# Optimization experiments

Measured on AMD Instinct MI355X. Metric: run time of the kernel, lower is better.

Reference implementation:

```python
import jax, jax.numpy as jnp
import numpy as np

B, N, D, H = 4, 2048, 256, 8
d = D // H          # 32 per-head dim
EPS = 1e-5
SCALE = 1.0 / float(np.sqrt(d))


def setup_inputs() -> dict:
    key = jax.random.key(0)
    ks = jax.random.split(key, 6)
    s = 0.02
    x = jax.random.normal(ks[0], (B, N, D), jnp.float32)
    # RoPE frequencies: theta_j = 10000^(-2j/d), angle = pos * theta
    inv_freq = 1.0 / (10000.0 ** (jnp.arange(0, d, 2, dtype=jnp.float32) / d))  # (d/2,)
    ang = jnp.arange(N, dtype=jnp.float32)[:, None] * inv_freq[None, :]          # (N, d/2)
    return {
        "x": x,
        "freqs_cos": jnp.cos(ang),
        "freqs_sin": jnp.sin(ang),
        "w_qkv": jax.random.normal(ks[1], (D, 3 * D), jnp.float32) * s,
        "b_qkv": jnp.zeros((3 * D,), jnp.float32),
        "w_proj": jax.random.normal(ks[2], (D, D), jnp.float32) * s,
        "b_proj": jnp.zeros((D,), jnp.float32),
        "ln1_g": jnp.ones((D,), jnp.float32),
        "ln1_b": jnp.zeros((D,), jnp.float32),
        "ln2_g": jnp.ones((D,), jnp.float32),
        "ln2_b": jnp.zeros((D,), jnp.float32),
        "w1": jax.random.normal(ks[3], (D, 2 * D), jnp.float32) * s,
        "b1": jnp.zeros((2 * D,), jnp.float32),
        "w2": jax.random.normal(ks[4], (2 * D, D), jnp.float32) * s,
        "b2": jnp.zeros((D,), jnp.float32),
    }


def _layer_norm(x, g, b):
    mu = jnp.mean(x, axis=-1, keepdims=True)
    var = jnp.mean(jnp.square(x - mu), axis=-1, keepdims=True)
    return (x - mu) * jax.lax.rsqrt(var + EPS) * g + b


def _rope(t, cos, sin):
    # t: (B,H,N,d); interleaved (even,odd) pairs viewed as complex, multiplied by e^{i*ang}
    tr = t.reshape(B, H, N, d // 2, 2)
    te, to = tr[..., 0], tr[..., 1]
    c = cos[None, None, :, :]
    s = sin[None, None, :, :]
    oe = te * c - to * s
    oo = te * s + to * c
    return jnp.stack([oe, oo], axis=-1).reshape(B, H, N, d)


def reference(x, freqs_cos, freqs_sin, w_qkv, b_qkv, w_proj, b_proj,
              ln1_g, ln1_b, ln2_g, ln2_b, w1, b1, w2, b2):
    # Pre-LN MHSA with RoPE (dropout = identity at eval)
    h = _layer_norm(x, ln1_g, ln1_b)
    qkv = (h @ w_qkv + b_qkv).reshape(B, N, 3, H, d).transpose(0, 2, 3, 1, 4)  # (B,3,H,N,d)
    q, k, v = qkv[:, 0], qkv[:, 1], qkv[:, 2]
    q = _rope(q, freqs_cos, freqs_sin)
    k = _rope(k, freqs_cos, freqs_sin)
    attn = jax.nn.softmax(jnp.einsum('bhnd,bhmd->bhnm', q, k) * SCALE, axis=-1)
    out = jnp.einsum('bhnm,bhmd->bhnd', attn, v).transpose(0, 2, 1, 3).reshape(B, N, D)
    x = x + (out @ w_proj + b_proj)
    h = _layer_norm(x, ln2_g, ln2_b)
    ffn = jax.nn.relu(h @ w1 + b1) @ w2 + b2
    return x + ffn
```

## Files before the change

kernel.cpp:

```cpp
#include <hip/hip_runtime.h>
#include <hip/hip_bf16.h>
#include <math.h>

#define Bsz 4
#define Nseq 2048
#define Dm 256
#define Hh 8
#define Hd 32
#define EPS_ 1e-5f
#define SCALE_ 0.17677669529663687f
#define QSC_ (0.17677669529663687f * 1.4426950408889634f)

typedef __attribute__((ext_vector_type(8))) short short8;
typedef __attribute__((ext_vector_type(4))) short short4v;
typedef __attribute__((ext_vector_type(4))) float f32x4;
typedef __attribute__((ext_vector_type(16))) float f32x16;

__device__ __forceinline__ void gload16(const void* g, void* l) {
    __builtin_amdgcn_global_load_lds(
        (const __attribute__((address_space(1))) void*)g,
        (__attribute__((address_space(3))) void*)l, 16, 0, 0);
}

__device__ __forceinline__ short bf16s(float f) {
    __hip_bfloat16 h = __float2bfloat16(f);
    return *(short*)&h;
}

union FU { float f; unsigned u; };

__device__ __forceinline__ int pk2bf(float a, float b) {
    FU ua, ub; ua.f = a; ub.f = b;
    return (int)__builtin_amdgcn_perm(ub.u, ua.u, 0x07060302u);
}

union I4S8 { int i[4]; short8 s; };

__global__ __launch_bounds__(256) void ln_kernel(const float* __restrict__ x,
                                                 const float* __restrict__ g,
                                                 const float* __restrict__ b,
                                                 __hip_bfloat16* __restrict__ out) {
    int row  = blockIdx.x * 4 + (threadIdx.x >> 6);
    int lane = threadIdx.x & 63;
    const float* xr = x + (size_t)row * Dm;
    float4 v = *(const float4*)(xr + lane * 4);
    float s  = v.x + v.y + v.z + v.w;
    float ss = v.x * v.x + v.y * v.y + v.z * v.z + v.w * v.w;
    #pragma unroll
    for (int off = 32; off; off >>= 1) {
        s  += __shfl_xor(s, off);
        ss += __shfl_xor(ss, off);
    }
    float mu  = s * (1.0f / Dm);
    float var = ss * (1.0f / Dm) - mu * mu;
    float rs  = rsqrtf(var + EPS_);
    float4 gv = *(const float4*)(g + lane * 4);
    float4 bv = *(const float4*)(b + lane * 4);
    short4v o4 = { bf16s((v.x - mu) * rs * gv.x + bv.x),
                   bf16s((v.y - mu) * rs * gv.y + bv.y),
                   bf16s((v.z - mu) * rs * gv.z + bv.z),
                   bf16s((v.w - mu) * rs * gv.w + bv.w) };
    *(short4v*)(out + (size_t)row * Dm + lane * 4) = o4;
}

__global__ __launch_bounds__(256) void wconv_kernel(
    const float* __restrict__ s0, const float* __restrict__ s1,
    const float* __restrict__ s2, const float* __restrict__ s3,
    __hip_bfloat16* __restrict__ d0, __hip_bfloat16* __restrict__ d1,
    __hip_bfloat16* __restrict__ d2, __hip_bfloat16* __restrict__ d3) {
    __shared__ float t[32][33];
    int bid = blockIdx.x;
    const float* src; __hip_bfloat16* dst; int K, N, tb;
    if (bid < 192)      { src = s0; dst = d0; K = 256; N = 768; tb = bid; }
    else if (bid < 256) { src = s1; dst = d1; K = 256; N = 256; tb = bid - 192; }
    else if (bid < 384) { src = s2; dst = d2; K = 256; N = 512; tb = bid - 256; }
    else                { src = s3; dst = d3; K = 512; N = 256; tb = bid - 384; }
    int tn = N >> 5;
    int k0 = (tb / tn) * 32, n0 = (tb % tn) * 32;
    int c = threadIdx.x & 31, r0 = threadIdx.x >> 5;
    #pragma unroll
    for (int i = 0; i < 4; i++) {
        int r = r0 + i * 8;
        t[r][c] = src[(size_t)(k0 + r) * N + n0 + c];
    }
    __syncthreads();
    #pragma unroll
    for (int i = 0; i < 4; i++) {
        int n = r0 + i * 8;
        dst[(size_t)(n0 + n) * K + k0 + c] = __float2bfloat16(t[c][n]);
    }
}

template <int TM, int EPI>
__global__ __launch_bounds__(256) void mfma_gemm(const __hip_bfloat16* __restrict__ A,
                                                 const __hip_bfloat16* __restrict__ Wt,
                                                 const float* __restrict__ bias,
                                                 const float* __restrict__ res,
                                                 float* __restrict__ Cf,
                                                 __hip_bfloat16* __restrict__ Cb,
                                                 int M, int Nn, int K) {
    constexpr int MF = TM / 64;
    __shared__ __align__(16) __hip_bfloat16 As[TM * 32];
    __shared__ __align__(16) __hip_bfloat16 Bs[64 * 32];
    const int tid = threadIdx.x, w = tid >> 6, lane = tid & 63;
    const int lm = lane & 15, lq = lane >> 4;
    const int bm = blockIdx.y * TM, bn = blockIdx.x * 64;
    f32x4 acc[MF][4];
    #pragma unroll
    for (int i = 0; i < MF; i++)
        #pragma unroll
        for (int j = 0; j < 4; j++) acc[i][j] = (f32x4){0.f, 0.f, 0.f, 0.f};

    const int sw = (lq ^ (lm & 3)) * 8;
    for (int k0 = 0; k0 < K; k0 += 32) {
        #pragma unroll
        for (int p = 0; p < MF; p++) {
            int c = p * 256 + tid;
            int r = c >> 2, gk = ((c & 3) ^ (r & 3)) * 8;
            gload16(A + (size_t)(bm + r) * K + k0 + gk, As + (p * 256 + w * 64) * 8);
        }
        {
            int r = tid >> 2, gk = ((tid & 3) ^ (r & 3)) * 8;
            gload16(Wt + (size_t)(bn + r) * K + k0 + gk, Bs + w * 512);
        }
        __syncthreads();
        short8 a[MF];
        #pragma unroll
        for (int mf = 0; mf < MF; mf++)
            a[mf] = *(const short8*)&As[(w * (TM / 4) + mf * 16 + lm) * 32 + sw];
        #pragma unroll
        for (int nf = 0; nf < 4; nf++) {
            short8 bfr = *(const short8*)&Bs[(nf * 16 + lm) * 32 + sw];
            #pragma unroll
            for (int mf = 0; mf < MF; mf++)
                acc[mf][nf] = __builtin_amdgcn_mfma_f32_16x16x32_bf16(a[mf], bfr, acc[mf][nf], 0, 0, 0);
        }
        __syncthreads();
    }
    #pragma unroll
    for (int nf = 0; nf < 4; nf++) {
        int cg = bn + nf * 16 + lm;
        float bi = bias[cg];
        #pragma unroll
        for (int mf = 0; mf < MF; mf++) {
            #pragma unroll
            for (int r = 0; r < 4; r++) {
                int rg = bm + w * (TM / 4) + mf * 16 + lq * 4 + r;
                float v = acc[mf][nf][r] + bi;
                if (EPI == 1) {
                    v = fmaxf(v, 0.f);
                    Cb[(size_t)rg * Nn + cg] = __float2bfloat16(v);
                } else {
                    v += res[(size_t)rg * Nn + cg];
                    Cf[(size_t)rg * Nn + cg] = v;
                }
            }
        }
    }
}

__global__ __launch_bounds__(256) void qkv_mfma(const __hip_bfloat16* __restrict__ A,
                                                const __hip_bfloat16* __restrict__ Wt,
                                                const float* __restrict__ bias,
                                                const float* __restrict__ fcos,
                                                const float* __restrict__ fsin,
                                                __hip_bfloat16* __restrict__ qout,
                                                __hip_bfloat16* __restrict__ kout,
                                                __hip_bfloat16* __restrict__ vt) {
    const int K = 256, Nn = 768;
    __shared__ __align__(16) __hip_bfloat16 As[128 * 32];
    __shared__ __align__(16) __hip_bfloat16 Bs[64 * 32];
    const int tid = threadIdx.x, w = tid >> 6, lane = tid & 63;
    const int lm = lane & 15, lq = lane >> 4;
    const int bm = blockIdx.y * 128, bn = blockIdx.x * 64;
    f32x4 acc[2][4];
    #pragma unroll
    for (int i = 0; i < 2; i++)
        #pragma unroll
        for (int j = 0; j < 4; j++) acc[i][j] = (f32x4){0.f, 0.f, 0.f, 0.f};

    const int sw = (lq ^ (lm & 3)) * 8;
    for (int k0 = 0; k0 < K; k0 += 32) {
        #pragma unroll
        for (int p = 0; p < 2; p++) {
            int c = p * 256 + tid;
            int r = c >> 2, gk = ((c & 3) ^ (r & 3)) * 8;
            gload16(A + (size_t)(bm + r) * K + k0 + gk, As + (p * 256 + w * 64) * 8);
        }
        {
            int r = tid >> 2, gk = ((tid & 3) ^ (r & 3)) * 8;
            gload16(Wt + (size_t)(bn + r) * K + k0 + gk, Bs + w * 512);
        }
        __syncthreads();
        short8 a0 = *(const short8*)&As[(w * 32 + lm) * 32 + sw];
        short8 a1 = *(const short8*)&As[(w * 32 + 16 + lm) * 32 + sw];
        #pragma unroll
        for (int nf = 0; nf < 4; nf++) {
            short8 bfr = *(const short8*)&Bs[(nf * 16 + lm) * 32 + sw];
            acc[0][nf] = __builtin_amdgcn_mfma_f32_16x16x32_bf16(a0, bfr, acc[0][nf], 0, 0, 0);
            acc[1][nf] = __builtin_amdgcn_mfma_f32_16x16x32_bf16(a1, bfr, acc[1][nf], 0, 0, 0);
        }
        __syncthreads();
    }
    const int seg = bn >> 8;
    #pragma unroll
    for (int nf = 0; nf < 4; nf++) {
        int cg = bn + nf * 16 + lm;
        int hh = (cg & 255) >> 5;
        int dd = (nf & 1) * 16 + lm;
        int i0 = dd >> 1;
        float bi = bias[cg];
        #pragma unroll
        for (int mf = 0; mf < 2; mf++) {
            #pragma unroll
            for (int r = 0; r < 4; r++) {
                int rg = bm + w * 32 + mf * 16 + lq * 4 + r;
                int bb = rg >> 11, n = rg & (Nseq - 1);
                float v = acc[mf][nf][r] + bi;
                if (seg == 2) {
                    vt[(((size_t)(bb * Hh + hh)) * Hd + dd) * Nseq + n] = __float2bfloat16(v);
                } else {
                    float vp = __shfl_xor(v, 1);
                    float cs = fcos[n * 16 + i0], sn = fsin[n * 16 + i0];
                    float outv = (dd & 1) ? (vp * sn + v * cs) : (v * cs - vp * sn);
                    if (seg == 0) outv *= QSC_;
                    __hip_bfloat16* dst = (seg == 0) ? qout : kout;
                    dst[(((size_t)(bb * Hh + hh)) * Nseq + n) * Hd + dd] = __float2bfloat16(outv);
                }
            }
        }
    }
}

__global__ __launch_bounds__(256) void attn_mfma(const __hip_bfloat16* __restrict__ q,
                                                 const __hip_bfloat16* __restrict__ k,
                                                 const __hip_bfloat16* __restrict__ vt,
                                                 __hip_bfloat16* __restrict__ att) {
    __shared__ __align__(16) char smem[4096 + 16384 + 16384 + 512];
    __hip_bfloat16* Qs  = (__hip_bfloat16*)smem;
    __hip_bfloat16* KsB = (__hip_bfloat16*)(smem + 4096);
    __hip_bfloat16* VsB = (__hip_bfloat16*)(smem + 20480);
    float* RedO = (float*)(smem + 4096);
    float* RedS = (float*)(smem + 4096 + 8192);
    float* smS  = (float*)(smem + 4096 + 8192 + 256);

    const int tid = threadIdx.x, w = tid >> 6, lane = tid & 63;
    const int l31 = lane & 31, hi = lane >> 5;
    const int wq = w >> 1, wk = w & 1;
    const int bh = blockIdx.y, qbase = blockIdx.x * 64;
    const __hip_bfloat16* qp = q + ((size_t)bh * Nseq + qbase) * Hd;
    const __hip_bfloat16* kp = k + (size_t)bh * Nseq * Hd;
    const __hip_bfloat16* vp = vt + (size_t)bh * Hd * Nseq;
    const int r8 = tid >> 3, s8 = tid & 7;

    {
        int r = tid >> 2, sl = tid & 3;
        gload16(qp + r * 32 + ((sl ^ (r & 3)) * 8), Qs + w * 512);
    }
    #pragma unroll
    for (int par = 0; par < 2; par++) {
        gload16(kp + (par * 64 + 2 * r8 + (s8 >> 2)) * 32 + (((s8 & 3) ^ (r8 & 3)) * 8),
                KsB + par * 2048 + w * 512);
        gload16(vp + (size_t)r8 * Nseq + par * 64 + ((s8 ^ (r8 & 7)) * 8),
                VsB + par * 2048 + w * 512);
    }
    __syncthreads();

    const int qrow = wq * 32 + l31;
    short8 qf0 = *(const short8*)&Qs[qrow * 32 + ((hi ^ (l31 & 3)) * 8)];
    short8 qf1 = *(const short8*)&Qs[qrow * 32 + (((2 + hi) ^ (l31 & 3)) * 8)];

    f32x16 O;
    #pragma unroll
    for (int i = 0; i < 16; i++) O[i] = 0.f;
    float sm = 0.f;

    for (int t = 0; t < 16; t++) {
        const int buf = t & 1;
        if (t + 1 < 16) {
            const int kb2 = (t + 1) * 128;
            #pragma unroll
            for (int par = 0; par < 2; par++) {
                gload16(kp + (kb2 + par * 64 + 2 * r8 + (s8 >> 2)) * 32 + (((s8 & 3) ^ (r8 & 3)) * 8),
                        KsB + ((buf ^ 1) * 2 + par) * 2048 + w * 512);
                gload16(vp + (size_t)r8 * Nseq + kb2 + par * 64 + ((s8 ^ (r8 & 7)) * 8),
                        VsB + ((buf ^ 1) * 2 + par) * 2048 + w * 512);
            }
        }
        const __hip_bfloat16* Kc = KsB + (buf * 2 + wk) * 2048;
        const __hip_bfloat16* Vc = VsB + (buf * 2 + wk) * 2048;
        f32x16 St0, St1;
        #pragma unroll
        for (int i = 0; i < 16; i++) { St0[i] = 0.f; St1[i] = 0.f; }
        {
            int pr = l31 >> 1, elb = pr * 64 + (l31 & 1) * 32;
            short8 kf0 = *(const short8*)&Kc[elb + ((hi ^ (pr & 3)) * 8)];
            short8 kf1 = *(const short8*)&Kc[elb + (((2 + hi) ^ (pr & 3)) * 8)];
            St0 = __builtin_amdgcn_mfma_f32_32x32x16_bf16(kf0, qf0, St0, 0, 0, 0);
            St0 = __builtin_amdgcn_mfma_f32_32x32x16_bf16(kf1, qf1, St0, 0, 0, 0);
        }
        {
            int pr = 16 + (l31 >> 1), elb = pr * 64 + (l31 & 1) * 32;
            short8 kf0 = *(const short8*)&Kc[elb + ((hi ^ (pr & 3)) * 8)];
            short8 kf1 = *(const short8*)&Kc[elb + (((2 + hi) ^ (pr & 3)) * 8)];
            St1 = __builtin_amdgcn_mfma_f32_32x32x16_bf16(kf0, qf0, St1, 0, 0, 0);
            St1 = __builtin_amdgcn_mfma_f32_32x32x16_bf16(kf1, qf1, St1, 0, 0, 0);
        }
        int pk0[8], pk1[8];
        #pragma unroll
        for (int p = 0; p < 8; p++) {
            float a = __builtin_amdgcn_exp2f(St0[2 * p]);
            float b = __builtin_amdgcn_exp2f(St0[2 * p + 1]);
            sm += a + b;
            pk0[p] = pk2bf(a, b);
        }
        #pragma unroll
        for (int p = 0; p < 8; p++) {
            float a = __builtin_amdgcn_exp2f(St1[2 * p]);
            float b = __builtin_amdgcn_exp2f(St1[2 * p + 1]);
            sm += a + b;
            pk1[p] = pk2bf(a, b);
        }
        #pragma unroll
        for (int tt = 0; tt < 4; tt++) {
            const int* PK = (tt >> 1) ? pk1 : pk0;
            const int base = 4 * (tt & 1);
            int keep0 = hi ? PK[base + 2] : PK[base + 0];
            int keep1 = hi ? PK[base + 3] : PK[base + 1];
            int send0 = hi ? PK[base + 0] : PK[base + 2];
            int send1 = hi ? PK[base + 1] : PK[base + 3];
            int x0 = __shfl_xor(send0, 32);
            int x1 = __shfl_xor(send1, 32);
            I4S8 u;
            u.i[0] = hi ? x0 : keep0;
            u.i[1] = hi ? x1 : keep1;
            u.i[2] = hi ? keep0 : x0;
            u.i[3] = hi ? keep1 : x1;
            short8 vf = *(const short8*)&Vc[l31 * 64 + (((2 * tt + hi) ^ (l31 & 7)) * 8)];
            O = __builtin_amdgcn_mfma_f32_32x32x16_bf16(u.s, vf, O, 0, 0, 0);
        }
        __syncthreads();
    }
    sm += __shfl_xor(sm, 32);
    if (wk == 1) {
        #pragma unroll
        for (int j = 0; j < 16; j++) RedO[(wq * 16 + j) * 64 + lane] = O[j];
        if (hi == 0) RedS[wq * 32 + l31] = sm;
    }
    __syncthreads();
    if (wk == 0) {
        #pragma unroll
        for (int j = 0; j < 16; j++) O[j] += RedO[(wq * 16 + j) * 64 + lane];
        sm += RedS[wq * 32 + l31];
        if (hi == 0) smS[wq * 32 + l31] = sm;
    }
    __syncthreads();
    if (wk == 0) {
        const int bb = bh >> 3, hh = bh & 7;
        #pragma unroll
        for (int m = 0; m < 4; m++) {
            float4 sv = *(const float4*)&smS[wq * 32 + 8 * m + 4 * hi];
            #pragma unroll
            for (int i = 0; i < 4; i++) {
                int n = qbase + wq * 32 + 8 * m + 4 * hi + i;
                att[((size_t)(bb * Nseq + n)) * Dm + hh * Hd + l31] =
                    __float2bfloat16(O[4 * m + i] * (1.0f / sv[i]));
            }
        }
    }
}

extern "C" void kernel_launch(void* const* d_in, const int* in_sizes, int n_in,
                              void* d_out, int out_size, void* d_ws, size_t ws_size,
                              hipStream_t stream) {
    const float* x      = (const float*)d_in[0];
    const float* fcos   = (const float*)d_in[1];
    const float* fsin   = (const float*)d_in[2];
    const float* w_qkv  = (const float*)d_in[3];
    const float* b_qkv  = (const float*)d_in[4];
    const float* w_proj = (const float*)d_in[5];
    const float* b_proj = (const float*)d_in[6];
    const float* ln1_g  = (const float*)d_in[7];
    const float* ln1_b  = (const float*)d_in[8];
    const float* ln2_g  = (const float*)d_in[9];
    const float* ln2_b  = (const float*)d_in[10];
    const float* w1     = (const float*)d_in[11];
    const float* b1     = (const float*)d_in[12];
    const float* w2     = (const float*)d_in[13];
    const float* b2     = (const float*)d_in[14];
    float* out = (float*)d_out;
    char* base = (char*)d_ws;
    const size_t MB = (size_t)1 << 20;

    __hip_bfloat16* h   = (__hip_bfloat16*)(base);
    __hip_bfloat16* qb  = (__hip_bfloat16*)(base + 4 * MB);
    __hip_bfloat16* kbf = (__hip_bfloat16*)(base + 8 * MB);
    __hip_bfloat16* vtb = (__hip_bfloat16*)(base + 12 * MB);
    __hip_bfloat16* att = (__hip_bfloat16*)(base + 16 * MB);
    float*          x2f = (float*)(base + 20 * MB);
    __hip_bfloat16* h2  = (__hip_bfloat16*)(base);
    __hip_bfloat16* ffn = (__hip_bfloat16*)(base + 28 * MB);
    __hip_bfloat16* wqT = (__hip_bfloat16*)(base + 40 * MB);
    __hip_bfloat16* wpT = (__hip_bfloat16*)(base + 40 * MB + 393216);
    __hip_bfloat16* w1T = (__hip_bfloat16*)(base + 40 * MB + 524288);
    __hip_bfloat16* w2T = (__hip_bfloat16*)(base + 40 * MB + 786432);

    const int rows = Bsz * Nseq;

    wconv_kernel<<<512, 256, 0, stream>>>(w_qkv, w_proj, w1, w2, wqT, wpT, w1T, w2T);
    ln_kernel<<<rows / 4, 256, 0, stream>>>(x, ln1_g, ln1_b, h);
    qkv_mfma<<<dim3(12, 64), 256, 0, stream>>>(h, wqT, b_qkv, fcos, fsin, qb, kbf, vtb);
    attn_mfma<<<dim3(Nseq / 64, Bsz * Hh), 256, 0, stream>>>(qb, kbf, vtb, att);
    mfma_gemm<64, 2><<<dim3(4, 128), 256, 0, stream>>>(att, wpT, b_proj, x, x2f, nullptr,
                                                       rows, 256, 256);
    ln_kernel<<<rows / 4, 256, 0, stream>>>(x2f, ln2_g, ln2_b, h2);
    mfma_gemm<128, 1><<<dim3(8, 64), 256, 0, stream>>>(h2, w1T, b1, nullptr, nullptr, ffn,
                                                       rows, 512, 256);
    mfma_gemm<64, 2><<<dim3(4, 128), 256, 0, stream>>>(ffn, w2T, b2, x2f, out, nullptr,
                                                       rows, 256, 512);
}
```

Baseline: 184.5 us.

## Double-buffer GEMM LDS tiles with K=64 steps and fuse LN1 with weight conversion

Both GEMM kernels now take K-steps of 64 with double-buffered LDS tiles, an 8-way XOR swizzle and a single barrier per iteration. The next tile's loads are issued before the current tile's MFMAs, so global load latency can be hidden. The M tile is fixed at 64, which doubles the grid for the QKV and FFN1 GEMMs. The first LayerNorm and the weight transpose/convert kernel are merged into one launch to cut launch overhead. The trade-off is more LDS per block and less reuse of each weight tile across rows.

```diff
diff --git a/kernel.cpp b/kernel.cpp
--- a/kernel.cpp
+++ b/kernel.cpp
@@ -35,6 +35,60 @@
 }
 
 union I4S8 { int i[4]; short8 s; };
+
+__global__ __launch_bounds__(256) void prep_kernel(
+    const float* __restrict__ x, const float* __restrict__ g1,
+    const float* __restrict__ b1v, __hip_bfloat16* __restrict__ hout,
+    const float* __restrict__ s0, const float* __restrict__ s1,
+    const float* __restrict__ s2, const float* __restrict__ s3,
+    __hip_bfloat16* __restrict__ d0, __hip_bfloat16* __restrict__ d1,
+    __hip_bfloat16* __restrict__ d2, __hip_bfloat16* __restrict__ d3) {
+    __shared__ float t[32][33];
+    if (blockIdx.x < 2048) {
+        int row  = blockIdx.x * 4 + (threadIdx.x >> 6);
+        int lane = threadIdx.x & 63;
+        const float* xr = x + (size_t)row * Dm;
+        float4 v = *(const float4*)(xr + lane * 4);
+        float s  = v.x + v.y + v.z + v.w;
+        float ss = v.x * v.x + v.y * v.y + v.z * v.z + v.w * v.w;
+        #pragma unroll
+        for (int off = 32; off; off >>= 1) {
+            s  += __shfl_xor(s, off);
+            ss += __shfl_xor(ss, off);
+        }
+        float mu  = s * (1.0f / Dm);
+        float var = ss * (1.0f / Dm) - mu * mu;
+        float rs  = rsqrtf(var + EPS_);
+        float4 gv = *(const float4*)(g1 + lane * 4);
+        float4 bv = *(const float4*)(b1v + lane * 4);
+        short4v o4 = { bf16s((v.x - mu) * rs * gv.x + bv.x),
+                       bf16s((v.y - mu) * rs * gv.y + bv.y),
+                       bf16s((v.z - mu) * rs * gv.z + bv.z),
+                       bf16s((v.w - mu) * rs * gv.w + bv.w) };
+        *(short4v*)(hout + (size_t)row * Dm + lane * 4) = o4;
+        return;
+    }
+    int bid = blockIdx.x - 2048;
+    const float* src; __hip_bfloat16* dst; int K, N, tb;
+    if (bid < 192)      { src = s0; dst = d0; K = 256; N = 768; tb = bid; }
+    else if (bid < 256) { src = s1; dst = d1; K = 256; N = 256; tb = bid - 192; }
+    else if (bid < 384) { src = s2; dst = d2; K = 256; N = 512; tb = bid - 256; }
+    else                { src = s3; dst = d3; K = 512; N = 256; tb = bid - 384; }
+    int tn = N >> 5;
+    int k0 = (tb / tn) * 32, n0 = (tb % tn) * 32;
+    int c = threadIdx.x & 31, r0 = threadIdx.x >> 5;
+    #pragma unroll
+    for (int i = 0; i < 4; i++) {
+        int r = r0 + i * 8;
+        t[r][c] = src[(size_t)(k0 + r) * N + n0 + c];
+    }
+    __syncthreads();
+    #pragma unroll
+    for (int i = 0; i < 4; i++) {
+        int n = r0 + i * 8;
+        dst[(size_t)(n0 + n) * K + k0 + c] = __float2bfloat16(t[c][n]);
+    }
+}
 
 __global__ __launch_bounds__(256) void ln_kernel(const float* __restrict__ x,
                                                  const float* __restrict__ g,
@@ -63,35 +117,7 @@
     *(short4v*)(out + (size_t)row * Dm + lane * 4) = o4;
 }
 
-__global__ __launch_bounds__(256) void wconv_kernel(
-    const float* __restrict__ s0, const float* __restrict__ s1,
-    const float* __restrict__ s2, const float* __restrict__ s3,
-    __hip_bfloat16* __restrict__ d0, __hip_bfloat16* __restrict__ d1,
-    __hip_bfloat16* __restrict__ d2, __hip_bfloat16* __restrict__ d3) {
-    __shared__ float t[32][33];
-    int bid = blockIdx.x;
-    const float* src; __hip_bfloat16* dst; int K, N, tb;
-    if (bid < 192)      { src = s0; dst = d0; K = 256; N = 768; tb = bid; }
-    else if (bid < 256) { src = s1; dst = d1; K = 256; N = 256; tb = bid - 192; }
-    else if (bid < 384) { src = s2; dst = d2; K = 256; N = 512; tb = bid - 256; }
-    else                { src = s3; dst = d3; K = 512; N = 256; tb = bid - 384; }
-    int tn = N >> 5;
-    int k0 = (tb / tn) * 32, n0 = (tb % tn) * 32;
-    int c = threadIdx.x & 31, r0 = threadIdx.x >> 5;
-    #pragma unroll
-    for (int i = 0; i < 4; i++) {
-        int r = r0 + i * 8;
-        t[r][c] = src[(size_t)(k0 + r) * N + n0 + c];
-    }
-    __syncthreads();
-    #pragma unroll
-    for (int i = 0; i < 4; i++) {
-        int n = r0 + i * 8;
-        dst[(size_t)(n0 + n) * K + k0 + c] = __float2bfloat16(t[c][n]);
-    }
-}
-
-template <int TM, int EPI>
+template <int EPI>
 __global__ __launch_bounds__(256) void mfma_gemm(const __hip_bfloat16* __restrict__ A,
                                                  const __hip_bfloat16* __restrict__ Wt,
                                                  const float* __restrict__ bias,
@@ -99,61 +125,62 @@
                                                  float* __restrict__ Cf,
                                                  __hip_bfloat16* __restrict__ Cb,
                                                  int M, int Nn, int K) {
-    constexpr int MF = TM / 64;
-    __shared__ __align__(16) __hip_bfloat16 As[TM * 32];
-    __shared__ __align__(16) __hip_bfloat16 Bs[64 * 32];
+    __shared__ __align__(16) __hip_bfloat16 As[2][64 * 64];
+    __shared__ __align__(16) __hip_bfloat16 Bs[2][64 * 64];
     const int tid = threadIdx.x, w = tid >> 6, lane = tid & 63;
     const int lm = lane & 15, lq = lane >> 4;
-    const int bm = blockIdx.y * TM, bn = blockIdx.x * 64;
-    f32x4 acc[MF][4];
-    #pragma unroll
-    for (int i = 0; i < MF; i++)
-        #pragma unroll
-        for (int j = 0; j < 4; j++) acc[i][j] = (f32x4){0.f, 0.f, 0.f, 0.f};
-
-    const int sw = (lq ^ (lm & 3)) * 8;
-    for (int k0 = 0; k0 < K; k0 += 32) {
-        #pragma unroll
-        for (int p = 0; p < MF; p++) {
-            int c = p * 256 + tid;
-            int r = c >> 2, gk = ((c & 3) ^ (r & 3)) * 8;
-            gload16(A + (size_t)(bm + r) * K + k0 + gk, As + (p * 256 + w * 64) * 8);
-        }
-        {
-            int r = tid >> 2, gk = ((tid & 3) ^ (r & 3)) * 8;
-            gload16(Wt + (size_t)(bn + r) * K + k0 + gk, Bs + w * 512);
-        }
+    const int bm = blockIdx.y * 64, bn = blockIdx.x * 64;
+    f32x4 acc[4];
+    #pragma unroll
+    for (int j = 0; j < 4; j++) acc[j] = (f32x4){0.f, 0.f, 0.f, 0.f};
+
+    const int sr = tid >> 3, ssl = tid & 7;
+    const int sgk = (ssl ^ (sr & 7)) * 8;
+    const int sr2 = 32 + sr;
+    const int sgk2 = (ssl ^ (sr2 & 7)) * 8;
+
+    gload16(A + (size_t)(bm + sr) * K + sgk, &As[0][w * 512]);
+    gload16(A + (size_t)(bm + sr2) * K + sgk2, &As[0][2048 + w * 512]);
+    gload16(Wt + (size_t)(bn + sr) * K + sgk, &Bs[0][w * 512]);
+    gload16(Wt + (size_t)(bn + sr2) * K + sgk2, &Bs[0][2048 + w * 512]);
+
+    const int arow = w * 16 + lm;
+    const int ar7 = arow & 7, cr7base = lm & 7;
+    for (int t = 0; t < K / 64; t++) {
+        const int buf = t & 1;
         __syncthreads();
-        short8 a[MF];
-        #pragma unroll
-        for (int mf = 0; mf < MF; mf++)
-            a[mf] = *(const short8*)&As[(w * (TM / 4) + mf * 16 + lm) * 32 + sw];
-        #pragma unroll
-        for (int nf = 0; nf < 4; nf++) {
-            short8 bfr = *(const short8*)&Bs[(nf * 16 + lm) * 32 + sw];
+        if (t + 1 < K / 64) {
+            int k0 = (t + 1) * 64;
+            gload16(A + (size_t)(bm + sr) * K + k0 + sgk, &As[buf ^ 1][w * 512]);
+            gload16(A + (size_t)(bm + sr2) * K + k0 + sgk2, &As[buf ^ 1][2048 + w * 512]);
+            gload16(Wt + (size_t)(bn + sr) * K + k0 + sgk, &Bs[buf ^ 1][w * 512]);
+            gload16(Wt + (size_t)(bn + sr2) * K + k0 + sgk2, &Bs[buf ^ 1][2048 + w * 512]);
+        }
+        #pragma unroll
+        for (int ks = 0; ks < 2; ks++) {
+            short8 a = *(const short8*)&As[buf][arow * 64 + (((ks * 4 + lq) ^ ar7) * 8)];
             #pragma unroll
-            for (int mf = 0; mf < MF; mf++)
-                acc[mf][nf] = __builtin_amdgcn_mfma_f32_16x16x32_bf16(a[mf], bfr, acc[mf][nf], 0, 0, 0);
-        }
-        __syncthreads();
+            for (int nf = 0; nf < 4; nf++) {
+                int cc = nf * 16 + lm;
+                short8 bfr = *(const short8*)&Bs[buf][cc * 64 + (((ks * 4 + lq) ^ (cc & 7)) * 8)];
+                acc[nf] = __builtin_amdgcn_mfma_f32_16x16x32_bf16(a, bfr, acc[nf], 0, 0, 0);
+            }
+        }
     }
     #pragma unroll
     for (int nf = 0; nf < 4; nf++) {
         int cg = bn + nf * 16 + lm;
         float bi = bias[cg];
         #pragma unroll
-        for (int mf = 0; mf < MF; mf++) {
-            #pragma unroll
-            for (int r = 0; r < 4; r++) {
-                int rg = bm + w * (TM / 4) + mf * 16 + lq * 4 + r;
-                float v = acc[mf][nf][r] + bi;
-                if (EPI == 1) {
-                    v = fmaxf(v, 0.f);
-                    Cb[(size_t)rg * Nn + cg] = __float2bfloat16(v);
-                } else {
-                    v += res[(size_t)rg * Nn + cg];
-                    Cf[(size_t)rg * Nn + cg] = v;
-                }
+        for (int r = 0; r < 4; r++) {
+            int rg = bm + w * 16 + lq * 4 + r;
+            float v = acc[nf][r] + bi;
+            if (EPI == 1) {
+                v = fmaxf(v, 0.f);
+                Cb[(size_t)rg * Nn + cg] = __float2bfloat16(v);
+            } else {
+                v += res[(size_t)rg * Nn + cg];
+                Cf[(size_t)rg * Nn + cg] = v;
             }
         }
     }
@@ -167,40 +194,48 @@
                                                 __hip_bfloat16* __restrict__ qout,
                                                 __hip_bfloat16* __restrict__ kout,
                                                 __hip_bfloat16* __restrict__ vt) {
-    const int K = 256, Nn = 768;
-    __shared__ __align__(16) __hip_bfloat16 As[128 * 32];
-    __shared__ __align__(16) __hip_bfloat16 Bs[64 * 32];
+    const int K = 256;
+    __shared__ __align__(16) __hip_bfloat16 As[2][64 * 64];
+    __shared__ __align__(16) __hip_bfloat16 Bs[2][64 * 64];
     const int tid = threadIdx.x, w = tid >> 6, lane = tid & 63;
     const int lm = lane & 15, lq = lane >> 4;
-    const int bm = blockIdx.y * 128, bn = blockIdx.x * 64;
-    f32x4 acc[2][4];
-    #pragma unroll
-    for (int i = 0; i < 2; i++)
-        #pragma unroll
-        for (int j = 0; j < 4; j++) acc[i][j] = (f32x4){0.f, 0.f, 0.f, 0.f};
-
-    const int sw = (lq ^ (lm & 3)) * 8;
-    for (int k0 = 0; k0 < K; k0 += 32) {
-        #pragma unroll
-        for (int p = 0; p < 2; p++) {
-            int c = p * 256 + tid;
-            int r = c >> 2, gk = ((c & 3) ^ (r & 3)) * 8;
-            gload16(A + (size_t)(bm + r) * K + k0 + gk, As + (p * 256 + w * 64) * 8);
-        }
-        {
-            int r = tid >> 2, gk = ((tid & 3) ^ (r & 3)) * 8;
-            gload16(Wt + (size_t)(bn + r) * K + k0 + gk, Bs + w * 512);
-        }
+    const int bm = blockIdx.y * 64, bn = blockIdx.x * 64;
+    f32x4 acc[4];
+    #pragma unroll
+    for (int j = 0; j < 4; j++) acc[j] = (f32x4){0.f, 0.f, 0.f, 0.f};
+
+    const int sr = tid >> 3, ssl = tid & 7;
+    const int sgk = (ssl ^ (sr & 7)) * 8;
+    const int sr2 = 32 + sr;
+    const int sgk2 = (ssl ^ (sr2 & 7)) * 8;
+
+    gload16(A + (size_t)(bm + sr) * K + sgk, &As[0][w * 512]);
+    gload16(A + (size_t)(bm + sr2) * K + sgk2, &As[0][2048 + w * 512]);
+    gload16(Wt + (size_t)(bn + sr) * K + sgk, &Bs[0][w * 512]);
+    gload16(Wt + (size_t)(bn + sr2) * K + sgk2, &Bs[0][2048 + w * 512]);
+
+    const int arow = w * 16 + lm;
+    const int ar7 = arow & 7;
+    for (int t = 0; t < K / 64; t++) {
+        const int buf = t & 1;
         __syncthreads();
-        short8 a0 = *(const short8*)&As[(w * 32 + lm) * 32 + sw];
-        short8 a1 = *(const short8*)&As[(w * 32 + 16 + lm) * 32 + sw];
-        #pragma unroll
-        for (int nf = 0; nf < 4; nf++) {
-            short8 bfr = *(const short8*)&Bs[(nf * 16 + lm) * 32 + sw];
-            acc[0][nf] = __builtin_amdgcn_mfma_f32_16x16x32_bf16(a0, bfr, acc[0][nf], 0, 0, 0);
-            acc[1][nf] = __builtin_amdgcn_mfma_f32_16x16x32_bf16(a1, bfr, acc[1][nf], 0, 0, 0);
-        }
-        __syncthreads();
+        if (t + 1 < K / 64) {
+            int k0 = (t + 1) * 64;
+            gload16(A + (size_t)(bm + sr) * K + k0 + sgk, &As[buf ^ 1][w * 512]);
+            gload16(A + (size_t)(bm + sr2) * K + k0 + sgk2, &As[buf ^ 1][2048 + w * 512]);
+            gload16(Wt + (size_t)(bn + sr) * K + k0 + sgk, &Bs[buf ^ 1][w * 512]);
+            gload16(Wt + (size_t)(bn + sr2) * K + k0 + sgk2, &Bs[buf ^ 1][2048 + w * 512]);
+        }
+        #pragma unroll
+        for (int ks = 0; ks < 2; ks++) {
+            short8 a = *(const short8*)&As[buf][arow * 64 + (((ks * 4 + lq) ^ ar7) * 8)];
+            #pragma unroll
+            for (int nf = 0; nf < 4; nf++) {
+                int cc = nf * 16 + lm;
+                short8 bfr = *(const short8*)&Bs[buf][cc * 64 + (((ks * 4 + lq) ^ (cc & 7)) * 8)];
+                acc[nf] = __builtin_amdgcn_mfma_f32_16x16x32_bf16(a, bfr, acc[nf], 0, 0, 0);
+            }
+        }
     }
     const int seg = bn >> 8;
     #pragma unroll
@@ -211,22 +246,19 @@
         int i0 = dd >> 1;
         float bi = bias[cg];
         #pragma unroll
-        for (int mf = 0; mf < 2; mf++) {
-            #pragma unroll
-            for (int r = 0; r < 4; r++) {
-                int rg = bm + w * 32 + mf * 16 + lq * 4 + r;
-                int bb = rg >> 11, n = rg & (Nseq - 1);
-                float v = acc[mf][nf][r] + bi;
-                if (seg == 2) {
-                    vt[(((size_t)(bb * Hh + hh)) * Hd + dd) * Nseq + n] = __float2bfloat16(v);
-                } else {
-                    float vp = __shfl_xor(v, 1);
-                    float cs = fcos[n * 16 + i0], sn = fsin[n * 16 + i0];
-                    float outv = (dd & 1) ? (vp * sn + v * cs) : (v * cs - vp * sn);
-                    if (seg == 0) outv *= QSC_;
-                    __hip_bfloat16* dst = (seg == 0) ? qout : kout;
-                    dst[(((size_t)(bb * Hh + hh)) * Nseq + n) * Hd + dd] = __float2bfloat16(outv);
-                }
+        for (int r = 0; r < 4; r++) {
+            int rg = bm + w * 16 + lq * 4 + r;
+            int bb = rg >> 11, n = rg & (Nseq - 1);
+            float v = acc[nf][r] + bi;
+            if (seg == 2) {
+                vt[(((size_t)(bb * Hh + hh)) * Hd + dd) * Nseq + n] = __float2bfloat16(v);
+            } else {
+                float vp = __shfl_xor(v, 1);
+                float cs = fcos[n * 16 + i0], sn = fsin[n * 16 + i0];
+                float outv = (dd & 1) ? (vp * sn + v * cs) : (v * cs - vp * sn);
+                if (seg == 0) outv *= QSC_;
+                __hip_bfloat16* dst = (seg == 0) ? qout : kout;
+                dst[(((size_t)(bb * Hh + hh)) * Nseq + n) * Hd + dd] = __float2bfloat16(outv);
             }
         }
     }
@@ -407,15 +439,15 @@
 
     const int rows = Bsz * Nseq;
 
-    wconv_kernel<<<512, 256, 0, stream>>>(w_qkv, w_proj, w1, w2, wqT, wpT, w1T, w2T);
-    ln_kernel<<<rows / 4, 256, 0, stream>>>(x, ln1_g, ln1_b, h);
-    qkv_mfma<<<dim3(12, 64), 256, 0, stream>>>(h, wqT, b_qkv, fcos, fsin, qb, kbf, vtb);
+    prep_kernel<<<2560, 256, 0, stream>>>(x, ln1_g, ln1_b, h,
+                                          w_qkv, w_proj, w1, w2, wqT, wpT, w1T, w2T);
+    qkv_mfma<<<dim3(12, 128), 256, 0, stream>>>(h, wqT, b_qkv, fcos, fsin, qb, kbf, vtb);
     attn_mfma<<<dim3(Nseq / 64, Bsz * Hh), 256, 0, stream>>>(qb, kbf, vtb, att);
-    mfma_gemm<64, 2><<<dim3(4, 128), 256, 0, stream>>>(att, wpT, b_proj, x, x2f, nullptr,
-                                                       rows, 256, 256);
+    mfma_gemm<2><<<dim3(4, 128), 256, 0, stream>>>(att, wpT, b_proj, x, x2f, nullptr,
+                                                   rows, 256, 256);
     ln_kernel<<<rows / 4, 256, 0, stream>>>(x2f, ln2_g, ln2_b, h2);
-    mfma_gemm<128, 1><<<dim3(8, 64), 256, 0, stream>>>(h2, w1T, b1, nullptr, nullptr, ffn,
-                                                       rows, 512, 256);
-    mfma_gemm<64, 2><<<dim3(4, 128), 256, 0, stream>>>(ffn, w2T, b2, x2f, out, nullptr,
-                                                       rows, 256, 512);
-}
+    mfma_gemm<1><<<dim3(8, 128), 256, 0, stream>>>(h2, w1T, b1, nullptr, nullptr, ffn,
+                                                   rows, 512, 256);
+    mfma_gemm<2><<<dim3(4, 128), 256, 0, stream>>>(ffn, w2T, b2, x2f, out, nullptr,
+                                                   rows, 256, 512);
+}
```

After: 174.2 us. -5.6%, faster.
